# Performance work log

Hardware: AMD Instinct MI355X
Metric: run time of the kernel (lower is better)

Reference implementation:

```python
import jax, jax.numpy as jnp
import numpy as np

B, S, D = 2, 2048, 1024
N, H = 16, 64  # n_heads, d_head
INIT_STD = 0.02
IGNORE = -100000.0


def setup_inputs() -> dict:
    key = jax.random.key(0)
    ks = jax.random.split(key, 6)
    return {
        "normalized_resid_pre": jax.random.normal(ks[0], (B, S, D), dtype=jnp.float32),
        "W_Q": jax.random.normal(ks[1], (N, D, H), dtype=jnp.float32) * INIT_STD,
        "W_K": jax.random.normal(ks[2], (N, D, H), dtype=jnp.float32) * INIT_STD,
        "W_V": jax.random.normal(ks[3], (N, D, H), dtype=jnp.float32) * INIT_STD,
        "W_O": jax.random.normal(ks[4], (N, H, D), dtype=jnp.float32) * INIT_STD,
        "b_Q": jnp.zeros((N, H), dtype=jnp.float32),
        "b_K": jnp.zeros((N, H), dtype=jnp.float32),
        "b_V": jnp.zeros((N, H), dtype=jnp.float32),
        "b_O": jnp.zeros((D,), dtype=jnp.float32),
    }


def reference(normalized_resid_pre, W_Q, W_K, W_V, W_O, b_Q, b_K, b_V, b_O):
    x = normalized_resid_pre
    q = jnp.einsum('ndh,bpd->bpnh', W_Q, x) + b_Q
    k = jnp.einsum('ndh,bpd->bpnh', W_K, x) + b_K
    v = jnp.einsum('ndh,bpd->bpnh', W_V, x) + b_V
    scores = jnp.einsum('bpnh,bsnh->bnps', q, k) / jnp.sqrt(jnp.float32(H))
    # causal mask: key_pos > query_pos -> IGNORE
    seq = scores.shape[-1]
    mask = jnp.triu(jnp.ones((seq, seq), dtype=bool), k=1)
    scores = jnp.where(mask, jnp.float32(IGNORE), scores)
    attn = jax.nn.softmax(scores, axis=-1)
    z = jnp.einsum('bnps,bsnh->bpnh', attn, v)
    # per-head out-proj then sum over heads
    out = jnp.einsum('bpnh,nhd->bpd', z, W_O) + b_O
    return out
```

## Files before the change

kernel.cpp:

```cpp
#include <hip/hip_runtime.h>
#include <math.h>

#define S_ 2048
#define D_ 1024
#define M_ 4096

typedef float f4 __attribute__((ext_vector_type(4)));
typedef float f16v __attribute__((ext_vector_type(16)));
typedef short s8v __attribute__((ext_vector_type(8)));
typedef unsigned short u16;

#define MFMA32(a,b,c) __builtin_amdgcn_mfma_f32_32x32x16_bf16((a),(b),(c),0,0,0)
#define QSCALE 0.1803368801111204f
#define NINF  -1e30f

__device__ __forceinline__ u16 f2bf(float x) {
    unsigned int u = __float_as_uint(x);
    u += 0x7fffu + ((u >> 16) & 1u);
    return (u16)(u >> 16);
}
__device__ __forceinline__ unsigned int cvtpk(float lo, float hi) {
    unsigned int r;
    asm("v_cvt_pk_bf16_f32 %0, %1, %2" : "=v"(r) : "v"(lo), "v"(hi));
    return r;
}
__device__ __forceinline__ void gload16(const void* g, void* l) {
    __builtin_amdgcn_global_load_lds(
        (const __attribute__((address_space(1))) unsigned int*)g,
        (__attribute__((address_space(3))) unsigned int*)l, 16, 0, 0);
}
union FragU { unsigned int u[4]; s8v v; };

__global__ __launch_bounds__(256) void cvt_x(const float* __restrict__ x,
                                             u16* __restrict__ xb)
{
    int i = (blockIdx.x * 256 + threadIdx.x) * 8;
    f4 a = *(const f4*)(x + i);
    f4 b = *(const f4*)(x + i + 4);
    unsigned long long p0 =
        (unsigned long long)f2bf(a[0]) | ((unsigned long long)f2bf(a[1]) << 16) |
        ((unsigned long long)f2bf(a[2]) << 32) | ((unsigned long long)f2bf(a[3]) << 48);
    unsigned long long p1 =
        (unsigned long long)f2bf(b[0]) | ((unsigned long long)f2bf(b[1]) << 16) |
        ((unsigned long long)f2bf(b[2]) << 32) | ((unsigned long long)f2bf(b[3]) << 48);
    *(unsigned long long*)(xb + i)     = p0;
    *(unsigned long long*)(xb + i + 4) = p1;
}

__global__ __launch_bounds__(256) void transW_kernel(
    const float* __restrict__ Wq, const float* __restrict__ Wk, const float* __restrict__ Wv,
    u16* __restrict__ Wc)
{
    const int which = blockIdx.z, n = blockIdx.y, dt = blockIdx.x;
    const float* W = which == 0 ? Wq : (which == 1 ? Wk : Wv);
    __shared__ float t[64][65];
    const int tid = threadIdx.x;
    #pragma unroll
    for (int it = 0; it < 4; ++it) {
        int c = tid + it * 256;
        int d = c >> 4, h4 = c & 15;
        f4 v = *(const f4*)(W + ((size_t)n * 1024 + dt * 64 + d) * 64 + h4 * 4);
        #pragma unroll
        for (int j = 0; j < 4; ++j) t[h4 * 4 + j][d] = v[j];
    }
    __syncthreads();
    #pragma unroll
    for (int it = 0; it < 4; ++it) {
        int c = tid + it * 256;
        int h = c >> 4, d4 = c & 15;
        size_t o = (size_t)(which * 1024 + n * 64 + h) * 1024 + dt * 64 + d4 * 4;
        *(unsigned long long*)(Wc + o) =
            (unsigned long long)f2bf(t[h][d4 * 4 + 0]) |
            ((unsigned long long)f2bf(t[h][d4 * 4 + 1]) << 16) |
            ((unsigned long long)f2bf(t[h][d4 * 4 + 2]) << 32) |
            ((unsigned long long)f2bf(t[h][d4 * 4 + 3]) << 48);
    }
}

__global__ __launch_bounds__(256) void transWo_kernel(
    const float* __restrict__ Wo, u16* __restrict__ WoT)
{
    const int rt = blockIdx.y, ct = blockIdx.x;
    __shared__ float t[64][65];
    const int tid = threadIdx.x;
    #pragma unroll
    for (int it = 0; it < 4; ++it) {
        int c = tid + it * 256;
        int r = c >> 4, c4 = c & 15;
        f4 v = *(const f4*)(Wo + (size_t)(rt * 64 + r) * 1024 + ct * 64 + c4 * 4);
        #pragma unroll
        for (int j = 0; j < 4; ++j) t[c4 * 4 + j][r] = v[j];
    }
    __syncthreads();
    #pragma unroll
    for (int it = 0; it < 4; ++it) {
        int c = tid + it * 256;
        int d = c >> 4, r4 = c & 15;
        size_t o = (size_t)(ct * 64 + d) * 1024 + rt * 64 + r4 * 4;
        *(unsigned long long*)(WoT + o) =
            (unsigned long long)f2bf(t[d][r4 * 4 + 0]) |
            ((unsigned long long)f2bf(t[d][r4 * 4 + 1]) << 16) |
            ((unsigned long long)f2bf(t[d][r4 * 4 + 2]) << 32) |
            ((unsigned long long)f2bf(t[d][r4 * 4 + 3]) << 48);
    }
}

__global__ void bcat_kernel(const float* bq, const float* bk, const float* bv, float* bc)
{
    int i = blockIdx.x * 256 + threadIdx.x;
    bc[i] = i < 1024 ? bq[i] : (i < 2048 ? bk[i - 1024] : bv[i - 2048]);
}

template<int MODE>
__global__ __launch_bounds__(256) void gemm_bf16(
    const u16* __restrict__ A, const u16* __restrict__ B,
    const float* __restrict__ bias,
    u16* __restrict__ outq, u16* __restrict__ outk, u16* __restrict__ outvT,
    float* __restrict__ outf)
{
    __shared__ u16 sm[16384];
    u16* Ash = sm;
    u16* Bsh = sm + 8192;

    const int tid = threadIdx.x;
    const int lane = tid & 63, w = tid >> 6;
    const int wm = w & 1, wn = w >> 1;
    const int l31 = lane & 31, hi = lane >> 5;
    const int m0 = blockIdx.x * 128, n0 = blockIdx.y * 128;
    const int srow = lane >> 3;
    const int sc8 = (lane & 7) ^ srow;
    const int rx = l31 & 7;

    f16v acc[2][2];
    #pragma unroll
    for (int a = 0; a < 2; ++a)
        #pragma unroll
        for (int b = 0; b < 2; ++b)
            #pragma unroll
            for (int r = 0; r < 16; ++r) acc[a][b][r] = 0.f;

    for (int kt = 0; kt < 16; ++kt) {
        __syncthreads();
        #pragma unroll
        for (int i = 0; i < 4; ++i) {
            const int rb = (i * 4 + w) * 8;
            const int row = rb + srow;
            gload16(A + (size_t)(m0 + row) * 1024 + kt * 64 + sc8 * 8, Ash + rb * 64);
            gload16(B + (size_t)(n0 + row) * 1024 + kt * 64 + sc8 * 8, Bsh + rb * 64);
        }
        __syncthreads();
        #pragma unroll
        for (int ks = 0; ks < 4; ++ks) {
            s8v af[2], bf[2];
            #pragma unroll
            for (int mb = 0; mb < 2; ++mb)
                af[mb] = *(const s8v*)&Ash[(64 * wm + 32 * mb + l31) * 64 +
                                           ((2 * ks + hi) ^ rx) * 8];
            #pragma unroll
            for (int nb = 0; nb < 2; ++nb)
                bf[nb] = *(const s8v*)&Bsh[(64 * wn + 32 * nb + l31) * 64 +
                                           ((2 * ks + hi) ^ rx) * 8];
            #pragma unroll
            for (int mb = 0; mb < 2; ++mb)
                #pragma unroll
                for (int nb = 0; nb < 2; ++nb)
                    acc[mb][nb] = MFMA32(af[mb], bf[nb], acc[mb][nb]);
        }
    }

    __syncthreads();

    if constexpr (MODE == 0) {
        u16* Zw = sm + w * 4096;
        const int which = n0 >> 10;
        #pragma unroll
        for (int nb = 0; nb < 2; ++nb) {
            int nhl = 32 * nb + l31;
            float bv = bias[n0 + 64 * wn + nhl];
            #pragma unroll
            for (int mb = 0; mb < 2; ++mb)
                #pragma unroll
                for (int r = 0; r < 16; ++r) {
                    int ml = 32 * mb + (r & 3) + 8 * (r >> 2) + 4 * hi;
                    float vv = acc[mb][nb][r] + bv;
                    if (which == 0) vv *= QSCALE;
                    u16 hv = f2bf(vv);
                    int idx = (which == 2)
                        ? nhl * 64 + (ml ^ ((nhl & 7) << 3))
                        : ml * 64 + (nhl ^ ((ml & 7) << 3));
                    Zw[idx] = hv;
                }
        }
        __syncthreads();
        const int gmb = m0 + 64 * wm;
        const int gnb = n0 + 64 * wn;
        #pragma unroll
        for (int it = 0; it < 8; ++it) {
            int c = lane + it * 64;
            int row = c >> 3, c8 = c & 7;
            int idx = row * 64 + 8 * (c8 ^ (row & 7));
            s8v val = *(const s8v*)&Zw[idx];
            if (which == 0)
                *(s8v*)(outq + (size_t)(gmb + row) * 1024 + gnb + c8 * 8) = val;
            else if (which == 1)
                *(s8v*)(outk + (size_t)(gmb + row) * 1024 + (gnb - 1024) + c8 * 8) = val;
            else
                *(s8v*)(outvT + (size_t)(gnb - 2048 + row) * 4096 + gmb + c8 * 8) = val;
        }
    } else {
        #pragma unroll
        for (int nb = 0; nb < 2; ++nb) {
            int gcol = n0 + 64 * wn + 32 * nb + l31;
            float bv = bias[gcol];
            #pragma unroll
            for (int mb = 0; mb < 2; ++mb)
                #pragma unroll
                for (int r = 0; r < 16; ++r) {
                    int gm = m0 + 64 * wm + 32 * mb + (r & 3) + 8 * (r >> 2) + 4 * hi;
                    outf[(size_t)gm * 1024 + gcol] = acc[mb][nb][r] + bv;
                }
        }
    }
}

__global__ __launch_bounds__(256) void attn_mfma(
    const u16* __restrict__ qp, const u16* __restrict__ kp,
    const u16* __restrict__ vTp, u16* __restrict__ zp)
{
    __shared__ u16 sm[16384];
    const int tid = threadIdx.x;
    const int lane = tid & 63, w = tid >> 6;
    const int l31 = lane & 31, hi = lane >> 5;
    const int qt = (int)gridDim.x - 1 - (int)blockIdx.x;
    const int n = blockIdx.y, b = blockIdx.z;
    const int q0 = qt * 128;
    const int qrow = q0 + 32 * w + l31;
    const int wqmin = q0 + 32 * w, wqmax = wqmin + 31;
    const size_t mrow = (size_t)b * 2048 + qrow;
    const int srow = lane >> 3;
    const int sc8 = (lane & 7) ^ srow;
    const int rx = l31 & 7;

    s8v qf[4];
    #pragma unroll
    for (int c = 0; c < 4; ++c)
        qf[c] = *(const s8v*)(qp + mrow * 1024 + n * 64 + c * 16 + hi * 8);

    f16v acc[2];
    #pragma unroll
    for (int mb = 0; mb < 2; ++mb)
        #pragma unroll
        for (int r = 0; r < 16; ++r) acc[mb][r] = 0.f;
    float mrun = NINF, lrun = 0.f;
    const int nkt = 2 * qt + 2;

    auto STAGE = [&](int kt, int bufi) {
        u16* Kd = sm + bufi * 8192;
        u16* Vd = Kd + 4096;
        #pragma unroll
        for (int i = 0; i < 2; ++i) {
            const int rb = (i * 4 + w) * 8;
            const int row = rb + srow;
            gload16(kp + ((size_t)b * 2048 + kt * 64 + row) * 1024 + n * 64 + sc8 * 8,
                    Kd + rb * 64);
            gload16(vTp + ((size_t)n * 64 + row) * 4096 + b * 2048 + kt * 64 + sc8 * 8,
                    Vd + rb * 64);
        }
    };

    STAGE(0, 0);
    int cur = 0;
    for (int kt = 0; kt < nkt; ++kt) {
        __syncthreads();
        if (kt + 1 < nkt) STAGE(kt + 1, cur ^ 1);
        if (64 * kt <= wqmax) {
            const u16* Kd = sm + cur * 8192;
            const u16* Vd = Kd + 4096;

            f16v sf[2];
            #pragma unroll
            for (int t = 0; t < 2; ++t) {
                #pragma unroll
                for (int r = 0; r < 16; ++r) sf[t][r] = 0.f;
                const int row = 32 * t + l31;
                #pragma unroll
                for (int c = 0; c < 4; ++c) {
                    s8v kf = *(const s8v*)&Kd[row * 64 + ((2 * c + hi) ^ rx) * 8];
                    sf[t] = MFMA32(kf, qf[c], sf[t]);
                }
            }

            if (64 * kt + 63 > wqmin) {
                #pragma unroll
                for (int t = 0; t < 2; ++t)
                    #pragma unroll
                    for (int r = 0; r < 16; ++r) {
                        const int sg = kt * 64 + 32 * t + (r & 3) + 8 * (r >> 2) + 4 * hi;
                        if (sg > qrow) sf[t][r] = NINF;
                    }
            }

            float ma = NINF, mb2 = NINF, mc = NINF, md = NINF;
            #pragma unroll
            for (int t = 0; t < 2; ++t)
                #pragma unroll
                for (int r = 0; r < 16; r += 4) {
                    ma  = fmaxf(ma,  sf[t][r]);
                    mb2 = fmaxf(mb2, sf[t][r + 1]);
                    mc  = fmaxf(mc,  sf[t][r + 2]);
                    md  = fmaxf(md,  sf[t][r + 3]);
                }
            float mloc = fmaxf(fmaxf(ma, mb2), fmaxf(mc, md));
            mloc = fmaxf(mloc, __shfl_xor(mloc, 32, 64));

            float mbase;
            bool defer = (mloc - mrun <= 8.0f);
            if (__all(defer)) {
                mbase = mrun;
            } else {
                float mnew = fmaxf(mrun, mloc);
                float alpha = exp2f(mrun - mnew);
                lrun *= alpha;
                #pragma unroll
                for (int mb = 0; mb < 2; ++mb)
                    #pragma unroll
                    for (int r = 0; r < 16; ++r) acc[mb][r] *= alpha;
                mrun = mnew;
                mbase = mnew;
            }
            float sa = 0.f, sb = 0.f, sc2 = 0.f, sd = 0.f;
            #pragma unroll
            for (int t = 0; t < 2; ++t)
                #pragma unroll
                for (int r = 0; r < 16; r += 4) {
                    float p0 = exp2f(sf[t][r]     - mbase);
                    float p1 = exp2f(sf[t][r + 1] - mbase);
                    float p2 = exp2f(sf[t][r + 2] - mbase);
                    float p3 = exp2f(sf[t][r + 3] - mbase);
                    sf[t][r] = p0; sf[t][r + 1] = p1;
                    sf[t][r + 2] = p2; sf[t][r + 3] = p3;
                    sa += p0; sb += p1; sc2 += p2; sd += p3;
                }
            float ls = (sa + sb) + (sc2 + sd);
            ls += __shfl_xor(ls, 32, 64);
            lrun += ls;

            s8v pf[4];
            #pragma unroll
            for (int c = 0; c < 4; ++c) {
                const int i0 = 2 * c, i1 = 2 * c + 1;
                const int t0 = i0 >> 2, u0 = i0 & 3;
                const int t1 = i1 >> 2, u1 = i1 & 3;
                unsigned int f00 = cvtpk(sf[t0][4 * u0 + 0], sf[t0][4 * u0 + 1]);
                unsigned int f01 = cvtpk(sf[t0][4 * u0 + 2], sf[t0][4 * u0 + 3]);
                unsigned int f10 = cvtpk(sf[t1][4 * u1 + 0], sf[t1][4 * u1 + 1]);
                unsigned int f11 = cvtpk(sf[t1][4 * u1 + 2], sf[t1][4 * u1 + 3]);
                unsigned int s0 = hi ? f00 : f10, s1 = hi ? f01 : f11;
                unsigned int r0 = __shfl_xor(s0, 32, 64);
                unsigned int r1 = __shfl_xor(s1, 32, 64);
                FragU f;
                f.u[0] = hi ? r0 : f00;  f.u[1] = hi ? r1 : f01;
                f.u[2] = hi ? f10 : r0;  f.u[3] = hi ? f11 : r1;
                pf[c] = f.v;
            }

            #pragma unroll
            for (int mb = 0; mb < 2; ++mb) {
                const int row = 32 * mb + l31;
                #pragma unroll
                for (int c = 0; c < 4; ++c) {
                    s8v vf = *(const s8v*)&Vd[row * 64 + ((2 * c + hi) ^ rx) * 8];
                    acc[mb] = MFMA32(vf, pf[c], acc[mb]);
                }
            }
        }
        cur ^= 1;
    }

    __syncthreads();
    float linv = 1.0f / lrun;
    u16* Z = sm + w * 2048;
    #pragma unroll
    for (int mb = 0; mb < 2; ++mb)
        #pragma unroll
        for (int r = 0; r < 16; ++r) {
            int hcol = 32 * mb + (r & 3) + 8 * (r >> 2) + 4 * hi;
            int idx = l31 * 64 + (hcol ^ ((l31 & 7) << 3));
            Z[idx] = f2bf(acc[mb][r] * linv);
        }
    __syncthreads();
    #pragma unroll
    for (int it = 0; it < 4; ++it) {
        int c = lane + it * 64;
        int row = c >> 3, c8 = c & 7;
        int idx = row * 64 + 8 * (c8 ^ (row & 7));
        *(s8v*)(zp + ((size_t)b * 2048 + q0 + 32 * w + row) * 1024 + n * 64 + c8 * 8) =
            *(const s8v*)&Z[idx];
    }
}

extern "C" void kernel_launch(void* const* d_in, const int* in_sizes, int n_in,
                              void* d_out, int out_size, void* d_ws, size_t ws_size,
                              hipStream_t stream) {
    const float* x  = (const float*)d_in[0];
    const float* Wq = (const float*)d_in[1];
    const float* Wk = (const float*)d_in[2];
    const float* Wv = (const float*)d_in[3];
    const float* Wo = (const float*)d_in[4];
    const float* bq = (const float*)d_in[5];
    const float* bk = (const float*)d_in[6];
    const float* bv = (const float*)d_in[7];
    const float* bO = (const float*)d_in[8];
    float* out = (float*)d_out;

    char* p = (char*)d_ws;
    size_t o = 0;
    auto alloc = [&](size_t bytes) { char* r = p + o; o += bytes; return r; };
    const size_t MB8 = (size_t)M_ * D_ * 2;
    u16* xb   = (u16*)alloc(MB8);
    u16* Wc   = (u16*)alloc((size_t)3072 * 1024 * 2);
    u16* WoT  = (u16*)alloc((size_t)1024 * 1024 * 2);
    float* bc = (float*)alloc(65536);
    u16* qb   = (u16*)alloc(MB8);
    u16* kb   = (u16*)alloc(MB8);
    u16* vTb  = (u16*)alloc(MB8);
    if (ws_size < o) return;
    u16* zb = xb;

    cvt_x<<<2048, 256, 0, stream>>>(x, xb);
    transW_kernel<<<dim3(16, 16, 3), 256, 0, stream>>>(Wq, Wk, Wv, Wc);
    transWo_kernel<<<dim3(16, 16), 256, 0, stream>>>(Wo, WoT);
    bcat_kernel<<<12, 256, 0, stream>>>(bq, bk, bv, bc);
    gemm_bf16<0><<<dim3(32, 24), 256, 0, stream>>>(
        xb, Wc, bc, qb, kb, vTb, nullptr);
    attn_mfma<<<dim3(16, 16, 2), 256, 0, stream>>>(qb, kb, vTb, zb);
    gemm_bf16<1><<<dim3(32, 8), 256, 0, stream>>>(
        zb, WoT, bO, nullptr, nullptr, nullptr, out);
}
```

Baseline: 231.2 us.

## Fuse prep kernels and retile attention to 64-row query blocks with XCD swizzle

Result: slower. 248.4 us (+7.4%).

```diff
diff --git a/kernel.cpp b/kernel.cpp
--- a/kernel.cpp
+++ b/kernel.cpp
@@ -31,84 +31,81 @@
 }
 union FragU { unsigned int u[4]; s8v v; };
 
-__global__ __launch_bounds__(256) void cvt_x(const float* __restrict__ x,
-                                             u16* __restrict__ xb)
+__global__ __launch_bounds__(256) void prep_fused(
+    const float* __restrict__ x,
+    const float* __restrict__ Wq, const float* __restrict__ Wk, const float* __restrict__ Wv,
+    const float* __restrict__ Wo,
+    const float* __restrict__ bq, const float* __restrict__ bk, const float* __restrict__ bv,
+    u16* __restrict__ xb, u16* __restrict__ Wc, u16* __restrict__ WoT,
+    float* __restrict__ bc)
 {
-    int i = (blockIdx.x * 256 + threadIdx.x) * 8;
-    f4 a = *(const f4*)(x + i);
-    f4 b = *(const f4*)(x + i + 4);
-    unsigned long long p0 =
-        (unsigned long long)f2bf(a[0]) | ((unsigned long long)f2bf(a[1]) << 16) |
-        ((unsigned long long)f2bf(a[2]) << 32) | ((unsigned long long)f2bf(a[3]) << 48);
-    unsigned long long p1 =
-        (unsigned long long)f2bf(b[0]) | ((unsigned long long)f2bf(b[1]) << 16) |
-        ((unsigned long long)f2bf(b[2]) << 32) | ((unsigned long long)f2bf(b[3]) << 48);
-    *(unsigned long long*)(xb + i)     = p0;
-    *(unsigned long long*)(xb + i + 4) = p1;
-}
-
-__global__ __launch_bounds__(256) void transW_kernel(
-    const float* __restrict__ Wq, const float* __restrict__ Wk, const float* __restrict__ Wv,
-    u16* __restrict__ Wc)
-{
-    const int which = blockIdx.z, n = blockIdx.y, dt = blockIdx.x;
-    const float* W = which == 0 ? Wq : (which == 1 ? Wk : Wv);
     __shared__ float t[64][65];
+    const int bid = blockIdx.x;
     const int tid = threadIdx.x;
-    #pragma unroll
-    for (int it = 0; it < 4; ++it) {
-        int c = tid + it * 256;
-        int d = c >> 4, h4 = c & 15;
-        f4 v = *(const f4*)(W + ((size_t)n * 1024 + dt * 64 + d) * 64 + h4 * 4);
-        #pragma unroll
-        for (int j = 0; j < 4; ++j) t[h4 * 4 + j][d] = v[j];
+
+    if (bid < 2048) {
+        int i = (bid * 256 + tid) * 8;
+        f4 a = *(const f4*)(x + i);
+        f4 b = *(const f4*)(x + i + 4);
+        unsigned long long p0 =
+            (unsigned long long)f2bf(a[0]) | ((unsigned long long)f2bf(a[1]) << 16) |
+            ((unsigned long long)f2bf(a[2]) << 32) | ((unsigned long long)f2bf(a[3]) << 48);
+        unsigned long long p1 =
+            (unsigned long long)f2bf(b[0]) | ((unsigned long long)f2bf(b[1]) << 16) |
+            ((unsigned long long)f2bf(b[2]) << 32) | ((unsigned long long)f2bf(b[3]) << 48);
+        *(unsigned long long*)(xb + i)     = p0;
+        *(unsigned long long*)(xb + i + 4) = p1;
+    } else if (bid < 2816) {
+        const int wb = bid - 2048;
+        const int which = wb >> 8, n = (wb >> 4) & 15, dt = wb & 15;
+        const float* W = which == 0 ? Wq : (which == 1 ? Wk : Wv);
+        #pragma unroll
+        for (int it = 0; it < 4; ++it) {
+            int c = tid + it * 256;
+            int d = c >> 4, h4 = c & 15;
+            f4 v = *(const f4*)(W + ((size_t)n * 1024 + dt * 64 + d) * 64 + h4 * 4);
+            #pragma unroll
+            for (int j = 0; j < 4; ++j) t[h4 * 4 + j][d] = v[j];
+        }
+        __syncthreads();
+        #pragma unroll
+        for (int it = 0; it < 4; ++it) {
+            int c = tid + it * 256;
+            int h = c >> 4, d4 = c & 15;
+            size_t o = (size_t)(which * 1024 + n * 64 + h) * 1024 + dt * 64 + d4 * 4;
+            *(unsigned long long*)(Wc + o) =
+                (unsigned long long)f2bf(t[h][d4 * 4 + 0]) |
+                ((unsigned long long)f2bf(t[h][d4 * 4 + 1]) << 16) |
+                ((unsigned long long)f2bf(t[h][d4 * 4 + 2]) << 32) |
+                ((unsigned long long)f2bf(t[h][d4 * 4 + 3]) << 48);
+        }
+    } else if (bid < 3072) {
+        const int ob = bid - 2816;
+        const int rt = ob >> 4, ct = ob & 15;
+        #pragma unroll
+        for (int it = 0; it < 4; ++it) {
+            int c = tid + it * 256;
+            int r = c >> 4, c4 = c & 15;
+            f4 v = *(const f4*)(Wo + (size_t)(rt * 64 + r) * 1024 + ct * 64 + c4 * 4);
+            #pragma unroll
+            for (int j = 0; j < 4; ++j) t[c4 * 4 + j][r] = v[j];
+        }
+        __syncthreads();
+        #pragma unroll
+        for (int it = 0; it < 4; ++it) {
+            int c = tid + it * 256;
+            int d = c >> 4, r4 = c & 15;
+            size_t o = (size_t)(ct * 64 + d) * 1024 + rt * 64 + r4 * 4;
+            *(unsigned long long*)(WoT + o) =
+                (unsigned long long)f2bf(t[d][r4 * 4 + 0]) |
+                ((unsigned long long)f2bf(t[d][r4 * 4 + 1]) << 16) |
+                ((unsigned long long)f2bf(t[d][r4 * 4 + 2]) << 32) |
+                ((unsigned long long)f2bf(t[d][r4 * 4 + 3]) << 48);
+        }
+    } else {
+        int i = (bid - 3072) * 256 + tid;
+        bc[i] = i < 1024 ? bq[i] : (i < 2048 ? bk[i - 1024] : bv[i - 2048]);
     }
-    __syncthreads();
-    #pragma unroll
-    for (int it = 0; it < 4; ++it) {
-        int c = tid + it * 256;
-        int h = c >> 4, d4 = c & 15;
-        size_t o = (size_t)(which * 1024 + n * 64 + h) * 1024 + dt * 64 + d4 * 4;
-        *(unsigned long long*)(Wc + o) =
-            (unsigned long long)f2bf(t[h][d4 * 4 + 0]) |
-            ((unsigned long long)f2bf(t[h][d4 * 4 + 1]) << 16) |
-            ((unsigned long long)f2bf(t[h][d4 * 4 + 2]) << 32) |
-            ((unsigned long long)f2bf(t[h][d4 * 4 + 3]) << 48);
-    }
-}
-
-__global__ __launch_bounds__(256) void transWo_kernel(
-    const float* __restrict__ Wo, u16* __restrict__ WoT)
-{
-    const int rt = blockIdx.y, ct = blockIdx.x;
-    __shared__ float t[64][65];
-    const int tid = threadIdx.x;
-    #pragma unroll
-    for (int it = 0; it < 4; ++it) {
-        int c = tid + it * 256;
-        int r = c >> 4, c4 = c & 15;
-        f4 v = *(const f4*)(Wo + (size_t)(rt * 64 + r) * 1024 + ct * 64 + c4 * 4);
-        #pragma unroll
-        for (int j = 0; j < 4; ++j) t[c4 * 4 + j][r] = v[j];
-    }
-    __syncthreads();
-    #pragma unroll
-    for (int it = 0; it < 4; ++it) {
-        int c = tid + it * 256;
-        int d = c >> 4, r4 = c & 15;
-        size_t o = (size_t)(ct * 64 + d) * 1024 + rt * 64 + r4 * 4;
-        *(unsigned long long*)(WoT + o) =
-            (unsigned long long)f2bf(t[d][r4 * 4 + 0]) |
-            ((unsigned long long)f2bf(t[d][r4 * 4 + 1]) << 16) |
-            ((unsigned long long)f2bf(t[d][r4 * 4 + 2]) << 32) |
-            ((unsigned long long)f2bf(t[d][r4 * 4 + 3]) << 48);
-    }
-}
-
-__global__ void bcat_kernel(const float* bq, const float* bk, const float* bv, float* bc)
-{
-    int i = blockIdx.x * 256 + threadIdx.x;
-    bc[i] = i < 1024 ? bq[i] : (i < 2048 ? bk[i - 1024] : bv[i - 2048]);
 }
 
 template<int MODE>
@@ -223,7 +220,7 @@
     }
 }
 
-__global__ __launch_bounds__(256) void attn_mfma(
+__global__ __launch_bounds__(128) void attn_mfma(
     const u16* __restrict__ qp, const u16* __restrict__ kp,
     const u16* __restrict__ vTp, u16* __restrict__ zp)
 {
@@ -231,11 +228,15 @@
     const int tid = threadIdx.x;
     const int lane = tid & 63, w = tid >> 6;
     const int l31 = lane & 31, hi = lane >> 5;
-    const int qt = (int)gridDim.x - 1 - (int)blockIdx.x;
-    const int n = blockIdx.y, b = blockIdx.z;
-    const int q0 = qt * 128;
+
+    const int bid = blockIdx.x;
+    const int lin = (bid & 7) * 128 + (bid >> 3);
+    const int qt = 31 - (lin & 31);
+    const int n = (lin >> 5) & 15, b = lin >> 9;
+
+    const int q0 = qt * 64;
     const int qrow = q0 + 32 * w + l31;
-    const int wqmin = q0 + 32 * w, wqmax = wqmin + 31;
+    const int wqmin = q0 + 32 * w;
     const size_t mrow = (size_t)b * 2048 + qrow;
     const int srow = lane >> 3;
     const int sc8 = (lane & 7) ^ srow;
@@ -252,14 +253,14 @@
         #pragma unroll
         for (int r = 0; r < 16; ++r) acc[mb][r] = 0.f;
     float mrun = NINF, lrun = 0.f;
-    const int nkt = 2 * qt + 2;
+    const int nkt = qt + 1;
 
     auto STAGE = [&](int kt, int bufi) {
         u16* Kd = sm + bufi * 8192;
         u16* Vd = Kd + 4096;
         #pragma unroll
-        for (int i = 0; i < 2; ++i) {
-            const int rb = (i * 4 + w) * 8;
+        for (int i = 0; i < 4; ++i) {
+            const int rb = (i * 2 + w) * 8;
             const int row = rb + srow;
             gload16(kp + ((size_t)b * 2048 + kt * 64 + row) * 1024 + n * 64 + sc8 * 8,
                     Kd + rb * 64);
@@ -273,107 +274,109 @@
     for (int kt = 0; kt < nkt; ++kt) {
         __syncthreads();
         if (kt + 1 < nkt) STAGE(kt + 1, cur ^ 1);
-        if (64 * kt <= wqmax) {
-            const u16* Kd = sm + cur * 8192;
-            const u16* Vd = Kd + 4096;
-
-            f16v sf[2];
-            #pragma unroll
-            for (int t = 0; t < 2; ++t) {
-                #pragma unroll
-                for (int r = 0; r < 16; ++r) sf[t][r] = 0.f;
-                const int row = 32 * t + l31;
-                #pragma unroll
-                for (int c = 0; c < 4; ++c) {
-                    s8v kf = *(const s8v*)&Kd[row * 64 + ((2 * c + hi) ^ rx) * 8];
-                    sf[t] = MFMA32(kf, qf[c], sf[t]);
-                }
+        const u16* Kd = sm + cur * 8192;
+        const u16* Vd = Kd + 4096;
+
+        f16v sf[2];
+        __builtin_amdgcn_s_setprio(1);
+        #pragma unroll
+        for (int t = 0; t < 2; ++t) {
+            #pragma unroll
+            for (int r = 0; r < 16; ++r) sf[t][r] = 0.f;
+            const int row = 32 * t + l31;
+            #pragma unroll
+            for (int c = 0; c < 4; ++c) {
+                s8v kf = *(const s8v*)&Kd[row * 64 + ((2 * c + hi) ^ rx) * 8];
+                sf[t] = MFMA32(kf, qf[c], sf[t]);
             }
-
-            if (64 * kt + 63 > wqmin) {
-                #pragma unroll
-                for (int t = 0; t < 2; ++t)
-                    #pragma unroll
-                    for (int r = 0; r < 16; ++r) {
-                        const int sg = kt * 64 + 32 * t + (r & 3) + 8 * (r >> 2) + 4 * hi;
-                        if (sg > qrow) sf[t][r] = NINF;
-                    }
-            }
-
-            float ma = NINF, mb2 = NINF, mc = NINF, md = NINF;
+        }
+        __builtin_amdgcn_s_setprio(0);
+
+        if (64 * kt + 63 > wqmin) {
             #pragma unroll
             for (int t = 0; t < 2; ++t)
                 #pragma unroll
-                for (int r = 0; r < 16; r += 4) {
-                    ma  = fmaxf(ma,  sf[t][r]);
-                    mb2 = fmaxf(mb2, sf[t][r + 1]);
-                    mc  = fmaxf(mc,  sf[t][r + 2]);
-                    md  = fmaxf(md,  sf[t][r + 3]);
+                for (int r = 0; r < 16; ++r) {
+                    const int sg = kt * 64 + 32 * t + (r & 3) + 8 * (r >> 2) + 4 * hi;
+                    if (sg > qrow) sf[t][r] = NINF;
                 }
-            float mloc = fmaxf(fmaxf(ma, mb2), fmaxf(mc, md));
-            mloc = fmaxf(mloc, __shfl_xor(mloc, 32, 64));
-
-            float mbase;
-            bool defer = (mloc - mrun <= 8.0f);
-            if (__all(defer)) {
-                mbase = mrun;
-            } else {
-                float mnew = fmaxf(mrun, mloc);
-                float alpha = exp2f(mrun - mnew);
-                lrun *= alpha;
+        }
+
+        float ma = NINF, mb2 = NINF, mc = NINF, md = NINF;
+        #pragma unroll
+        for (int t = 0; t < 2; ++t)
+            #pragma unroll
+            for (int r = 0; r < 16; r += 4) {
+                ma  = fmaxf(ma,  sf[t][r]);
+                mb2 = fmaxf(mb2, sf[t][r + 1]);
+                mc  = fmaxf(mc,  sf[t][r + 2]);
+                md  = fmaxf(md,  sf[t][r + 3]);
+            }
+        float mloc = fmaxf(fmaxf(ma, mb2), fmaxf(mc, md));
+        mloc = fmaxf(mloc, __shfl_xor(mloc, 32, 64));
+
+        float mbase;
+        bool defer = (mloc - mrun <= 8.0f);
+        if (__all(defer)) {
+            mbase = mrun;
+        } else {
+            float mnew = fmaxf(mrun, mloc);
+            float alpha = exp2f(mrun - mnew);
+            lrun *= alpha;
+            #pragma unroll
+            for (int mb = 0; mb < 2; ++mb)
                 #pragma unroll
-                for (int mb = 0; mb < 2; ++mb)
-                    #pragma unroll
-                    for (int r = 0; r < 16; ++r) acc[mb][r] *= alpha;
-                mrun = mnew;
-                mbase = mnew;
+                for (int r = 0; r < 16; ++r) acc[mb][r] *= alpha;
+            mrun = mnew;
+            mbase = mnew;
+        }
+        float sa = 0.f, sb = 0.f, sc2 = 0.f, sd = 0.f;
+        #pragma unroll
+        for (int t = 0; t < 2; ++t)
+            #pragma unroll
+            for (int r = 0; r < 16; r += 4) {
+                float p0 = exp2f(sf[t][r]     - mbase);
+                float p1 = exp2f(sf[t][r + 1] - mbase);
+                float p2 = exp2f(sf[t][r + 2] - mbase);
+                float p3 = exp2f(sf[t][r + 3] - mbase);
+                sf[t][r] = p0; sf[t][r + 1] = p1;
+                sf[t][r + 2] = p2; sf[t][r + 3] = p3;
+                sa += p0; sb += p1; sc2 += p2; sd += p3;
             }
-            float sa = 0.f, sb = 0.f, sc2 = 0.f, sd = 0.f;
-            #pragma unroll
-            for (int t = 0; t < 2; ++t)
-                #pragma unroll
-                for (int r = 0; r < 16; r += 4) {
-                    float p0 = exp2f(sf[t][r]     - mbase);
-                    float p1 = exp2f(sf[t][r + 1] - mbase);
-                    float p2 = exp2f(sf[t][r + 2] - mbase);
-                    float p3 = exp2f(sf[t][r + 3] - mbase);
-                    sf[t][r] = p0; sf[t][r + 1] = p1;
-                    sf[t][r + 2] = p2; sf[t][r + 3] = p3;
-                    sa += p0; sb += p1; sc2 += p2; sd += p3;
-                }
-            float ls = (sa + sb) + (sc2 + sd);
-            ls += __shfl_xor(ls, 32, 64);
-            lrun += ls;
-
-            s8v pf[4];
+        float ls = (sa + sb) + (sc2 + sd);
+        ls += __shfl_xor(ls, 32, 64);
+        lrun += ls;
+
+        s8v pf[4];
+        #pragma unroll
+        for (int c = 0; c < 4; ++c) {
+            const int i0 = 2 * c, i1 = 2 * c + 1;
+            const int t0 = i0 >> 2, u0 = i0 & 3;
+            const int t1 = i1 >> 2, u1 = i1 & 3;
+            unsigned int f00 = cvtpk(sf[t0][4 * u0 + 0], sf[t0][4 * u0 + 1]);
+            unsigned int f01 = cvtpk(sf[t0][4 * u0 + 2], sf[t0][4 * u0 + 3]);
+            unsigned int f10 = cvtpk(sf[t1][4 * u1 + 0], sf[t1][4 * u1 + 1]);
+            unsigned int f11 = cvtpk(sf[t1][4 * u1 + 2], sf[t1][4 * u1 + 3]);
+            unsigned int s0 = hi ? f00 : f10, s1 = hi ? f01 : f11;
+            unsigned int r0 = __shfl_xor(s0, 32, 64);
+            unsigned int r1 = __shfl_xor(s1, 32, 64);
+            FragU f;
+            f.u[0] = hi ? r0 : f00;  f.u[1] = hi ? r1 : f01;
+            f.u[2] = hi ? f10 : r0;  f.u[3] = hi ? f11 : r1;
+            pf[c] = f.v;
+        }
+
+        __builtin_amdgcn_s_setprio(1);
+        #pragma unroll
+        for (int mb = 0; mb < 2; ++mb) {
+            const int row = 32 * mb + l31;
             #pragma unroll
             for (int c = 0; c < 4; ++c) {
-                const int i0 = 2 * c, i1 = 2 * c + 1;
-                const int t0 = i0 >> 2, u0 = i0 & 3;
-                const int t1 = i1 >> 2, u1 = i1 & 3;
-                unsigned int f00 = cvtpk(sf[t0][4 * u0 + 0], sf[t0][4 * u0 + 1]);
-                unsigned int f01 = cvtpk(sf[t0][4 * u0 + 2], sf[t0][4 * u0 + 3]);
-                unsigned int f10 = cvtpk(sf[t1][4 * u1 + 0], sf[t1][4 * u1 + 1]);
-                unsigned int f11 = cvtpk(sf[t1][4 * u1 + 2], sf[t1][4 * u1 + 3]);
-                unsigned int s0 = hi ? f00 : f10, s1 = hi ? f01 : f11;
-                unsigned int r0 = __shfl_xor(s0, 32, 64);
-                unsigned int r1 = __shfl_xor(s1, 32, 64);
-                FragU f;
-                f.u[0] = hi ? r0 : f00;  f.u[1] = hi ? r1 : f01;
-                f.u[2] = hi ? f10 : r0;  f.u[3] = hi ? f11 : r1;
-                pf[c] = f.v;
+                s8v vf = *(const s8v*)&Vd[row * 64 + ((2 * c + hi) ^ rx) * 8];
+                acc[mb] = MFMA32(vf, pf[c], acc[mb]);
             }
-
-            #pragma unroll
-            for (int mb = 0; mb < 2; ++mb) {
-                const int row = 32 * mb + l31;
-                #pragma unroll
-                for (int c = 0; c < 4; ++c) {
-                    s8v vf = *(const s8v*)&Vd[row * 64 + ((2 * c + hi) ^ rx) * 8];
-                    acc[mb] = MFMA32(vf, pf[c], acc[mb]);
-                }
-            }
-        }
+        }
+        __builtin_amdgcn_s_setprio(0);
         cur ^= 1;
     }
 
@@ -427,13 +430,11 @@
     if (ws_size < o) return;
     u16* zb = xb;
 
-    cvt_x<<<2048, 256, 0, stream>>>(x, xb);
-    transW_kernel<<<dim3(16, 16, 3), 256, 0, stream>>>(Wq, Wk, Wv, Wc);
-    transWo_kernel<<<dim3(16, 16), 256, 0, stream>>>(Wo, WoT);
-    bcat_kernel<<<12, 256, 0, stream>>>(bq, bk, bv, bc);
+    prep_fused<<<3084, 256, 0, stream>>>(x, Wq, Wk, Wv, Wo, bq, bk, bv,
+                                         xb, Wc, WoT, bc);
     gemm_bf16<0><<<dim3(32, 24), 256, 0, stream>>>(
         xb, Wc, bc, qb, kb, vTb, nullptr);
-    attn_mfma<<<dim3(16, 16, 2), 256, 0, stream>>>(qb, kb, vTb, zb);
+    attn_mfma<<<1024, 128, 0, stream>>>(qb, kb, vTb, zb);
     gemm_bf16<1><<<dim3(32, 8), 256, 0, stream>>>(
         zb, WoT, bO, nullptr, nullptr, nullptr, out);
 }
```
